# Kernel optimization log

Measured on AMD Instinct MI355X. Metric: run time of the kernel, lower is better.

The kernel has to match this reference:

```python
import jax, jax.numpy as jnp
import numpy as np

EPS = 1e-5


def gather_nodes(nodes, idx):
    # nodes: [B,N,C], idx: [B,N,K] -> [B,N,K,C]
    return jax.vmap(lambda n, e: n[e])(nodes, idx)


def layer_norm(x, g, b):
    m = jnp.mean(x, axis=-1, keepdims=True)
    v = jnp.mean((x - m) ** 2, axis=-1, keepdims=True)
    return (x - m) * jax.lax.rsqrt(v + EPS) * g + b


def linear(x, W, b):
    return x @ W + b


def setup_inputs() -> dict:
    key = jax.random.key(0)
    B, N, K, H = 2, 2048, 48, 128
    ks = jax.random.split(key, 32)
    it = iter(range(32))
    def nrm(shape, scale=0.05):
        return jax.random.normal(ks[next(it)], shape, dtype=jnp.float32) * scale
    inp = {
        "h_V": nrm((B, N, H), 1.0),
        "h_V_atom": nrm((B, N, H), 1.0),
        "h_E": nrm((B, N, K, H), 1.0),
        # message MLP 1: in = H + 2*(H+H) = 5H = 640
        "W1": nrm((5 * H, H)), "b1": jnp.zeros((H,), jnp.float32),
        "W2": nrm((H, H)), "b2": jnp.zeros((H,), jnp.float32),
        "W3": nrm((H, H)), "b3": jnp.zeros((H,), jnp.float32),
        # message MLP 2: in = H + (H+H) = 3H = 384
        "W11": nrm((3 * H, H)), "b11": jnp.zeros((H,), jnp.float32),
        "W12": nrm((H, H)), "b12": jnp.zeros((H,), jnp.float32),
        "W13": nrm((H, H)), "b13": jnp.zeros((H,), jnp.float32),
        # FFN
        "W_in": nrm((H, 4 * H)), "b_in": jnp.zeros((4 * H,), jnp.float32),
        "W_out": nrm((4 * H, H)), "b_out": jnp.zeros((H,), jnp.float32),
        # LayerNorms
        "g1": jnp.ones((H,), jnp.float32), "be1": jnp.zeros((H,), jnp.float32),
        "g2": jnp.ones((H,), jnp.float32), "be2": jnp.zeros((H,), jnp.float32),
        "g3": jnp.ones((H,), jnp.float32), "be3": jnp.zeros((H,), jnp.float32),
        "mask_V": jnp.ones((B, N), jnp.float32),
        "mask_attend": jnp.ones((B, N, K), jnp.float32),
        "E_idx": jax.random.randint(ks[next(it)], (B, N, K), 0, N),
    }
    return inp


def reference(h_V, h_V_atom, h_E, W1, b1, W2, b2, W3, b3, W11, b11, W12, b12,
              W13, b13, W_in, b_in, W_out, b_out, g1, be1, g2, be2, g3, be3,
              mask_V, mask_attend, E_idx):
    gelu = lambda x: jax.nn.gelu(x, approximate=False)
    SCALE = 30.0
    K = h_E.shape[-2]

    # --- node message ---
    h_EV = jnp.concatenate([
        jnp.broadcast_to(h_V[:, :, None, :], h_E.shape[:3] + (h_V.shape[-1],)),
        h_E, gather_nodes(h_V, E_idx),
        h_E, gather_nodes(h_V_atom, E_idx),
    ], axis=-1)  # [B,N,K,5H]
    h_message = linear(gelu(linear(gelu(linear(h_EV, W1, b1)), W2, b2)), W3, b3)
    h_message = mask_attend[..., None] * h_message
    dh = jnp.sum(h_message, axis=-2) / SCALE
    h_V = layer_norm(h_V + dh, g1, be1)

    # --- FFN ---
    dh = linear(gelu(linear(h_V, W_in, b_in)), W_out, b_out)
    h_V = layer_norm(h_V + dh, g2, be2)
    h_V = mask_V[..., None] * h_V

    # --- edge update ---
    h_EV2 = jnp.concatenate([
        jnp.broadcast_to(h_V[:, :, None, :], h_E.shape[:3] + (h_V.shape[-1],)),
        h_E, gather_nodes(h_V, E_idx),
    ], axis=-1)  # [B,N,K,3H]
    h_message = linear(gelu(linear(gelu(linear(h_EV2, W11, b11)), W12, b12)), W13, b13)
    h_E = layer_norm(h_E + h_message, g3, be3)
    return (h_V, h_E)
```

## Files before the change

### kernel.cpp

```cpp
#include <hip/hip_runtime.h>
#include <hip/hip_bf16.h>

#define H 128
#define NN 2048
#define BB 2
#define EPSF 1e-5f

typedef __bf16 bf16;
typedef bf16 bf16x8 __attribute__((ext_vector_type(8)));
typedef bf16 bf16x4 __attribute__((ext_vector_type(4)));
typedef float f32x4 __attribute__((ext_vector_type(4)));
typedef float f32x2 __attribute__((ext_vector_type(2)));

#define U1_F     155648
#define U2_F     679936
#define HVMID_F  1204224
#define V2_F     1990656
#define V1_F     2252800
#define HVMID_B  3457024

__device__ __forceinline__ float gelu_f(float x) {
    float u = x * x;
    float p = __builtin_fmaf(u, 0.044715f, 1.0f);
    float w = x * p;
    float e = __builtin_amdgcn_exp2f(w * -2.3022083f);
    return x * __builtin_amdgcn_rcpf(1.0f + e);
}

#define MFMA16(a, b, c) __builtin_amdgcn_mfma_f32_16x16x32_bf16((a), (b), (c), 0, 0, 0)

#define GEMM_PIPE(U, A_EXPR, B0p, B1p, ACC)                                       \
    {                                                                             \
        bf16x8 bq0[3], bq1[3];                                                    \
        _Pragma("unroll")                                                         \
        for (int j = 0; j < 3 && j < (U); ++j) {                                  \
            bq0[j] = *(const bf16x8*)((B0p) + j * 32);                            \
            bq1[j] = *(const bf16x8*)((B1p) + j * 32);                            \
        }                                                                         \
        bf16x8 afc[3], afn[3];                                                    \
        _Pragma("unroll")                                                         \
        for (int rt = 0; rt < 3; ++rt) { const int u = 0; afc[rt] = (A_EXPR); }   \
        _Pragma("unroll")                                                         \
        for (int uu = 0; uu < (U); ++uu) {                                        \
            if (uu + 1 < (U)) {                                                   \
                _Pragma("unroll")                                                 \
                for (int rt = 0; rt < 3; ++rt) { const int u = uu + 1; afn[rt] = (A_EXPR); } \
            }                                                                     \
            __builtin_amdgcn_s_setprio(1);                                        \
            _Pragma("unroll")                                                     \
            for (int rt = 0; rt < 3; ++rt) {                                      \
                ACC[rt][0] = MFMA16(afc[rt], bq0[uu % 3], ACC[rt][0]);            \
                ACC[rt][1] = MFMA16(afc[rt], bq1[uu % 3], ACC[rt][1]);            \
            }                                                                     \
            __builtin_amdgcn_s_setprio(0);                                        \
            if (uu + 3 < (U)) {                                                   \
                bq0[uu % 3] = *(const bf16x8*)((B0p) + (uu + 3) * 32);            \
                bq1[uu % 3] = *(const bf16x8*)((B1p) + (uu + 3) * 32);            \
            }                                                                     \
            _Pragma("unroll")                                                     \
            for (int rt = 0; rt < 3; ++rt) afc[rt] = afn[rt];                     \
        }                                                                         \
    }

#define PACK_STORE(DST, ROW, PCOL, V0, V1)                                        \
    {                                                                             \
        union { bf16 h[2]; unsigned u; } pk_;                                     \
        pk_.h[0] = (V0); pk_.h[1] = (V1);                                         \
        *(unsigned*)&DST[ROW][PCOL] = pk_.u;                                      \
    }

__global__ void prep_weights(const float* __restrict__ W1, const float* __restrict__ W2,
                             const float* __restrict__ W3, const float* __restrict__ W11,
                             const float* __restrict__ W12, const float* __restrict__ W13,
                             const float* __restrict__ Win, const float* __restrict__ Wout,
                             bf16* __restrict__ ws)
{
    int i = blockIdx.x * 256 + threadIdx.x;
    float v;
    if (i < 65536) {
        int c = i >> 9, k = i & 511, s = k >> 7, k0 = k & 127;
        if (s == 0)      v = W1[k0 * H + c];
        else if (s == 1) {
            int klog = (k0 & ~31) + ((k0 & 1) << 4) + ((k0 & 31) >> 1);
            v = W1[(128 + klog) * H + c] + W1[(384 + klog) * H + c];
        }
        else if (s == 2) v = W1[(256 + k0) * H + c];
        else             v = W1[(512 + k0) * H + c];
    } else if (i < 81920)  { int j = i - 65536;  int c = j >> 7, p = j & 127;
                             int k = (p & ~31) + ((p & 1) << 4) + ((p & 31) >> 1);
                             v = W2[k * H + c]; }
    else if (i < 98304)    { int j = i - 81920;  int c = j >> 7, p = j & 127;
                             int k = (p & ~31) + ((p & 1) << 4) + ((p & 31) >> 1);
                             v = W3[k * H + c]; }
    else if (i < 147456)   { int j = i - 98304;  int c = j / 384, k = j - c * 384;
                             if (k >= 128 && k < 256) {
                                 int p = k - 128;
                                 int klog = (p & ~31) + ((p & 1) << 4) + ((p & 31) >> 1);
                                 v = W11[(128 + klog) * H + c];
                             } else {
                                 v = W11[k * H + c];
                             } }
    else if (i < 163840)   { int j = i - 147456; int c = j >> 7, p = j & 127;
                             int k = (p & ~31) + ((p & 1) << 4) + ((p & 31) >> 1);
                             v = W12[k * H + c]; }
    else if (i < 180224)   { int j = i - 163840; int c = j >> 7, p = j & 127;
                             int k = (p & ~31) + ((p & 1) << 4) + ((p & 31) >> 1);
                             v = W13[k * H + c]; }
    else if (i < 245760)   { int j = i - 180224; int jj = j >> 7, k = j & 127; v = Win[k * 512 + jj]; }
    else                   { int j = i - 245760; int c = j >> 9, k = j & 511; v = Wout[k * H + c]; }
    ws[i] = (bf16)v;
}

__global__ __launch_bounds__(512) void u1_kernel(
    const float* __restrict__ hV, const float* __restrict__ hVa,
    const float* __restrict__ b1, const bf16* __restrict__ ws, float* __restrict__ wsf)
{
    int n0 = blockIdx.x * 128;
    int t = threadIdx.x, w = t >> 6, l = t & 63, l16 = l & 15, lg = l >> 4;
    int wm = w >> 2, wn = w & 3;
    __shared__ __align__(16) bf16 sA[128][136];
    __shared__ __align__(16) bf16 sB[128][136];

    #pragma unroll
    for (int i = 0; i < 8; ++i) {
        int idx = t + i * 512;
        int row = idx >> 5, c4 = (idx & 31) << 2;
        f32x4 v = *(const f32x4*)(hV + (size_t)(n0 + row) * H + c4);
        bf16x4 o; o[0] = (bf16)v[0]; o[1] = (bf16)v[1]; o[2] = (bf16)v[2]; o[3] = (bf16)v[3];
        *(bf16x4*)(&sA[row][c4]) = o;
        f32x4 va = *(const f32x4*)(hVa + (size_t)(n0 + row) * H + c4);
        bf16x4 oa; oa[0] = (bf16)va[0]; oa[1] = (bf16)va[1]; oa[2] = (bf16)va[2]; oa[3] = (bf16)va[3];
        *(bf16x4*)(&sB[row][c4]) = oa;
    }
    __syncthreads();

    f32x4 accU[4][2], accV[4][2];
    #pragma unroll
    for (int rt = 0; rt < 4; ++rt)
        #pragma unroll
        for (int c2 = 0; c2 < 2; ++c2) {
            accU[rt][c2] = (f32x4){0.f, 0.f, 0.f, 0.f};
            accV[rt][c2] = (f32x4){0.f, 0.f, 0.f, 0.f};
        }
    #pragma unroll
    for (int kk = 0; kk < 4; ++kk) {
        bf16x8 af[4];
        #pragma unroll
        for (int rt = 0; rt < 4; ++rt)
            af[rt] = *(const bf16x8*)(&sA[wm * 64 + rt * 16 + l16][kk * 32 + lg * 8]);
        #pragma unroll
        for (int c2 = 0; c2 < 2; ++c2) {
            int c = wn * 32 + c2 * 16 + l16;
            bf16x8 bU = *(const bf16x8*)(&ws[(size_t)c * 512 + kk * 32 + lg * 8]);
            bf16x8 bV = *(const bf16x8*)(&ws[(size_t)c * 512 + 256 + kk * 32 + lg * 8]);
            #pragma unroll
            for (int rt = 0; rt < 4; ++rt) {
                accU[rt][c2] = MFMA16(af[rt], bU, accU[rt][c2]);
                accV[rt][c2] = MFMA16(af[rt], bV, accV[rt][c2]);
            }
        }
    }
    #pragma unroll
    for (int kk = 0; kk < 4; ++kk) {
        bf16x8 af[4];
        #pragma unroll
        for (int rt = 0; rt < 4; ++rt)
            af[rt] = *(const bf16x8*)(&sB[wm * 64 + rt * 16 + l16][kk * 32 + lg * 8]);
        #pragma unroll
        for (int c2 = 0; c2 < 2; ++c2) {
            int c = wn * 32 + c2 * 16 + l16;
            bf16x8 bV = *(const bf16x8*)(&ws[(size_t)c * 512 + 384 + kk * 32 + lg * 8]);
            #pragma unroll
            for (int rt = 0; rt < 4; ++rt)
                accV[rt][c2] = MFMA16(af[rt], bV, accV[rt][c2]);
        }
    }
    {
        int col0 = wn * 32 + l16, col1 = col0 + 16;
        int pcol = wn * 32 + l16 * 2;
        float bb0 = b1[col0], bb1 = b1[col1];
        #pragma unroll
        for (int rt = 0; rt < 4; ++rt)
            #pragma unroll
            for (int i = 0; i < 4; ++i) {
                int row = wm * 64 + rt * 16 + lg * 4 + i;
                f32x2 su; su[0] = accU[rt][0][i] + bb0; su[1] = accU[rt][1][i] + bb1;
                *(f32x2*)(wsf + U1_F + (size_t)(n0 + row) * H + pcol) = su;
                f32x2 sv; sv[0] = accV[rt][0][i]; sv[1] = accV[rt][1][i];
                *(f32x2*)(wsf + V1_F + (size_t)(n0 + row) * H + pcol) = sv;
            }
    }
}

__global__ __launch_bounds__(256, 4) void node_msg_kernel(
    const float* __restrict__ hV, const float* __restrict__ hE,
    const float* __restrict__ b2, const float* __restrict__ b3,
    const float* __restrict__ g1, const float* __restrict__ be1,
    const float* __restrict__ maskA, const int* __restrict__ Eidx,
    bf16* __restrict__ ws, float* __restrict__ wsf)
{
    __shared__ __align__(16) char smem[27136];
    bf16 (*sA)[136]  = (bf16(*)[136])smem;
    bf16 (*sH1)[136] = (bf16(*)[136])smem;
    bf16 (*sH2)[136] = (bf16(*)[136])(smem + 13056);
    float* sDH = (float*)(smem + 26112);

    int n = blockIdx.x, b = n >> 11;
    int t = threadIdx.x, w = t >> 6, l = t & 63, l16 = l & 15, lg = l >> 4;

    int col0 = w * 32 + l16, col1 = col0 + 16;
    int pcol = w * 32 + l16 * 2;
    f32x2 u1p = *(const f32x2*)(wsf + U1_F + (size_t)n * H + pcol);
    float b2v0 = b2[col0], b2v1 = b2[col1];
    float b3v0 = b3[col0], b3v1 = b3[col1];

    float v1v0[3][4], v1v1[3][4];
    #pragma unroll
    for (int rt = 0; rt < 3; ++rt)
        #pragma unroll
        for (int i = 0; i < 4; ++i) {
            int row = rt * 16 + lg * 4 + i;
            int nbr = Eidx[n * 48 + row];
            f32x2 vv = *(const f32x2*)(wsf + V1_F + ((size_t)b * NN + nbr) * H + pcol);
            v1v0[rt][i] = vv[0];
            v1v1[rt][i] = vv[1];
        }

    #pragma unroll
    for (int i = 0; i < 6; ++i) {
        int idx = t + i * 256;
        int row = idx >> 5, q = idx & 31;
        int c0 = (q >> 3) * 32 + (q & 7) * 2;
        const float* hp = hE + ((size_t)n * 48 + row) * H + c0;
        f32x2 a = *(const f32x2*)(hp);
        f32x2 c = *(const f32x2*)(hp + 16);
        bf16x4 o; o[0] = (bf16)a[0]; o[1] = (bf16)c[0]; o[2] = (bf16)a[1]; o[3] = (bf16)c[1];
        *(bf16x4*)(&sA[row][q * 4]) = o;
    }
    __syncthreads();

    f32x4 acc[3][2];
    #pragma unroll
    for (int rt = 0; rt < 3; ++rt)
        #pragma unroll
        for (int c2 = 0; c2 < 2; ++c2) acc[rt][c2] = (f32x4){0.f, 0.f, 0.f, 0.f};
    {
        const bf16* B0 = ws + (size_t)col0 * 512 + 128 + lg * 8;
        const bf16* B1 = ws + (size_t)col1 * 512 + 128 + lg * 8;
        GEMM_PIPE(4, (*(const bf16x8*)(&sA[rt * 16 + l16][u * 32 + lg * 8])), B0, B1, acc)
    }
    __syncthreads();

    #pragma unroll
    for (int rt = 0; rt < 3; ++rt)
        #pragma unroll
        for (int i = 0; i < 4; ++i) {
            int row = rt * 16 + lg * 4 + i;
            bf16 v0 = (bf16)gelu_f(acc[rt][0][i] + u1p[0] + v1v0[rt][i]);
            bf16 v1 = (bf16)gelu_f(acc[rt][1][i] + u1p[1] + v1v1[rt][i]);
            PACK_STORE(sH1, row, pcol, v0, v1)
        }
    __syncthreads();

    f32x4 a2[3][2];
    #pragma unroll
    for (int rt = 0; rt < 3; ++rt)
        #pragma unroll
        for (int c2 = 0; c2 < 2; ++c2) a2[rt][c2] = (f32x4){0.f, 0.f, 0.f, 0.f};
    {
        const bf16* B0 = ws + 65536 + (size_t)col0 * 128 + lg * 8;
        const bf16* B1 = ws + 65536 + (size_t)col1 * 128 + lg * 8;
        GEMM_PIPE(4, (*(const bf16x8*)(&sH1[rt * 16 + l16][u * 32 + lg * 8])), B0, B1, a2)
    }
    #pragma unroll
    for (int rt = 0; rt < 3; ++rt)
        #pragma unroll
        for (int i = 0; i < 4; ++i) {
            int row = rt * 16 + lg * 4 + i;
            bf16 v0 = (bf16)gelu_f(a2[rt][0][i] + b2v0);
            bf16 v1 = (bf16)gelu_f(a2[rt][1][i] + b2v1);
            PACK_STORE(sH2, row, pcol, v0, v1)
        }
    __syncthreads();

    float mk[3][4];
    #pragma unroll
    for (int rt = 0; rt < 3; ++rt)
        #pragma unroll
        for (int i = 0; i < 4; ++i)
            mk[rt][i] = maskA[n * 48 + rt * 16 + lg * 4 + i];

    f32x4 a3[3][2];
    #pragma unroll
    for (int rt = 0; rt < 3; ++rt)
        #pragma unroll
        for (int c2 = 0; c2 < 2; ++c2) a3[rt][c2] = (f32x4){0.f, 0.f, 0.f, 0.f};
    {
        const bf16* B0 = ws + 81920 + (size_t)col0 * 128 + lg * 8;
        const bf16* B1 = ws + 81920 + (size_t)col1 * 128 + lg * 8;
        GEMM_PIPE(4, (*(const bf16x8*)(&sH2[rt * 16 + l16][u * 32 + lg * 8])), B0, B1, a3)
    }
    float r0s = 0.f, r1s = 0.f;
    #pragma unroll
    for (int rt = 0; rt < 3; ++rt)
        #pragma unroll
        for (int i = 0; i < 4; ++i) {
            r0s += (a3[rt][0][i] + b3v0) * mk[rt][i];
            r1s += (a3[rt][1][i] + b3v1) * mk[rt][i];
        }
    r0s += __shfl_xor(r0s, 16); r0s += __shfl_xor(r0s, 32);
    r1s += __shfl_xor(r1s, 16); r1s += __shfl_xor(r1s, 32);
    if (l < 16) { sDH[w * 32 + l] = r0s; sDH[w * 32 + 16 + l] = r1s; }
    __syncthreads();

    if (w == 0) {
        float x0 = hV[(size_t)n * H + l] + sDH[l] * (1.0f / 30.0f);
        float x1 = hV[(size_t)n * H + l + 64] + sDH[l + 64] * (1.0f / 30.0f);
        float s1 = x0 + x1, s2 = x0 * x0 + x1 * x1;
        #pragma unroll
        for (int off = 32; off; off >>= 1) { s1 += __shfl_xor(s1, off); s2 += __shfl_xor(s2, off); }
        float m = s1 * (1.f / 128.f);
        float rs = rsqrtf(s2 * (1.f / 128.f) - m * m + EPSF);
        float y0 = (x0 - m) * rs * g1[l] + be1[l];
        float y1 = (x1 - m) * rs * g1[l + 64] + be1[l + 64];
        wsf[HVMID_F + (size_t)n * H + l] = y0;
        wsf[HVMID_F + (size_t)n * H + l + 64] = y1;
        ws[HVMID_B + (size_t)n * H + l] = (bf16)y0;
        ws[HVMID_B + (size_t)n * H + l + 64] = (bf16)y1;
    }
}

__global__ __launch_bounds__(512) void ffn_kernel(
    const float* __restrict__ b_in, const float* __restrict__ b_out,
    const float* __restrict__ b11, const float* __restrict__ g2,
    const float* __restrict__ be2, const float* __restrict__ maskV,
    bf16* __restrict__ ws, float* __restrict__ wsf, float* __restrict__ outV)
{
    int n0 = blockIdx.x * 32;
    int t = threadIdx.x, w = t >> 6, l = t & 63, l16 = l & 15, lg = l >> 4;

    __shared__ __align__(16) char smem[8704 + 33280];
    bf16 (*sA)[136]  = (bf16(*)[136])(smem);
    bf16 (*sFF)[520] = (bf16(*)[520])(smem + 8704);
    float (*sX)[132] = (float(*)[132])(smem + 8704);

    {
        int row = t >> 4, c8 = (t & 15) << 3;
        *(bf16x8*)(&sA[row][c8]) = *(const bf16x8*)(ws + HVMID_B + (size_t)(n0 + row) * H + c8);
    }
    __syncthreads();

    f32x4 a1[2][4];
    #pragma unroll
    for (int rt = 0; rt < 2; ++rt)
        #pragma unroll
        for (int ct = 0; ct < 4; ++ct) a1[rt][ct] = (f32x4){0.f, 0.f, 0.f, 0.f};
    #pragma unroll
    for (int kk = 0; kk < 4; ++kk) {
        bf16x8 af[2];
        #pragma unroll
        for (int rt = 0; rt < 2; ++rt)
            af[rt] = *(const bf16x8*)(&sA[rt * 16 + l16][kk * 32 + lg * 8]);
        #pragma unroll
        for (int ct = 0; ct < 4; ++ct) {
            int c = w * 64 + ct * 16 + l16;
            bf16x8 bfr = *(const bf16x8*)(&ws[180224 + (size_t)c * 128 + kk * 32 + lg * 8]);
            #pragma unroll
            for (int rt = 0; rt < 2; ++rt)
                a1[rt][ct] = MFMA16(af[rt], bfr, a1[rt][ct]);
        }
    }
    #pragma unroll
    for (int ct = 0; ct < 4; ++ct) {
        int c = w * 64 + ct * 16 + l16;
        float bb = b_in[c];
        #pragma unroll
        for (int rt = 0; rt < 2; ++rt)
            #pragma unroll
            for (int i = 0; i < 4; ++i) {
                int row = rt * 16 + lg * 4 + i;
                sFF[row][c] = (bf16)gelu_f(a1[rt][ct][i] + bb);
            }
    }
    __syncthreads();

    f32x4 a2[2];
    a2[0] = (f32x4){0.f, 0.f, 0.f, 0.f}; a2[1] = (f32x4){0.f, 0.f, 0.f, 0.f};
    int cc = w * 16 + l16;
    #pragma unroll
    for (int kk = 0; kk < 16; ++kk) {
        bf16x8 af[2];
        #pragma unroll
        for (int rt = 0; rt < 2; ++rt)
            af[rt] = *(const bf16x8*)(&sFF[rt * 16 + l16][kk * 32 + lg * 8]);
        bf16x8 bfr = *(const bf16x8*)(&ws[245760 + (size_t)cc * 512 + kk * 32 + lg * 8]);
        #pragma unroll
        for (int rt = 0; rt < 2; ++rt)
            a2[rt] = MFMA16(af[rt], bfr, a2[rt]);
    }
    __syncthreads();
    {
        float bb = b_out[cc];
        #pragma unroll
        for (int rt = 0; rt < 2; ++rt)
            #pragma unroll
            for (int i = 0; i < 4; ++i) {
                int row = rt * 16 + lg * 4 + i;
                sX[row][cc] = a2[rt][i] + bb + wsf[HVMID_F + (size_t)(n0 + row) * H + cc];
            }
    }
    __syncthreads();

    if (t < 128) {
        int row = t >> 2, q = t & 3;
        float xr[32], s1 = 0.f, s2 = 0.f;
        #pragma unroll
        for (int j = 0; j < 32; ++j) {
            float x = sX[row][q * 32 + j];
            xr[j] = x; s1 += x; s2 += x * x;
        }
        s1 += __shfl_xor(s1, 1); s1 += __shfl_xor(s1, 2);
        s2 += __shfl_xor(s2, 1); s2 += __shfl_xor(s2, 2);
        float m = s1 * (1.f / 128.f);
        float vv = s2 * (1.f / 128.f) - m * m;
        float rs = rsqrtf(vv + EPSF);
        float mv = maskV[n0 + row];
        #pragma unroll
        for (int j = 0; j < 32; ++j) {
            int c = q * 32 + j;
            float y = ((xr[j] - m) * rs * g2[c] + be2[c]) * mv;
            outV[(size_t)(n0 + row) * H + c] = y;
            sA[row][c] = (bf16)y;
        }
    }
    __syncthreads();

    f32x4 a3[2], a4[2];
    a3[0] = (f32x4){0.f, 0.f, 0.f, 0.f}; a3[1] = (f32x4){0.f, 0.f, 0.f, 0.f};
    a4[0] = (f32x4){0.f, 0.f, 0.f, 0.f}; a4[1] = (f32x4){0.f, 0.f, 0.f, 0.f};
    #pragma unroll
    for (int kk = 0; kk < 4; ++kk) {
        bf16x8 af[2];
        #pragma unroll
        for (int rt = 0; rt < 2; ++rt)
            af[rt] = *(const bf16x8*)(&sA[rt * 16 + l16][kk * 32 + lg * 8]);
        bf16x8 bU = *(const bf16x8*)(&ws[98304 + (size_t)cc * 384 + kk * 32 + lg * 8]);
        bf16x8 bV = *(const bf16x8*)(&ws[98304 + (size_t)cc * 384 + 256 + kk * 32 + lg * 8]);
        #pragma unroll
        for (int rt = 0; rt < 2; ++rt) {
            a3[rt] = MFMA16(af[rt], bU, a3[rt]);
            a4[rt] = MFMA16(af[rt], bV, a4[rt]);
        }
    }
    {
        float bb = b11[cc];
        int pc = (cc & ~31) + l16 * 2 + ((cc >> 4) & 1);
        #pragma unroll
        for (int rt = 0; rt < 2; ++rt)
            #pragma unroll
            for (int i = 0; i < 4; ++i) {
                int row = rt * 16 + lg * 4 + i;
                wsf[U2_F + (size_t)(n0 + row) * H + pc] = a3[rt][i] + bb;
                wsf[V2_F + (size_t)(n0 + row) * H + pc] = a4[rt][i];
            }
    }
}

__global__ __launch_bounds__(256, 4) void edge_kernel(
    const float* __restrict__ hE, const float* __restrict__ b12,
    const float* __restrict__ b13, const float* __restrict__ g3,
    const float* __restrict__ be3, const int* __restrict__ Eidx,
    const bf16* __restrict__ ws, const float* __restrict__ wsf,
    float* __restrict__ outE)
{
    __shared__ __align__(16) char smem[26112];
    bf16 (*sA)[136]  = (bf16(*)[136])smem;
    bf16 (*sH1)[136] = (bf16(*)[136])smem;
    bf16 (*sH2)[136] = (bf16(*)[136])(smem + 13056);
    float (*sP1)[4]  = (float(*)[4])smem;
    float (*sP2)[4]  = (float(*)[4])(smem + 1024);

    int n = blockIdx.x, b = n >> 11;
    int t = threadIdx.x, w = t >> 6, l = t & 63, l16 = l & 15, lg = l >> 4;

    int col0 = w * 32 + l16, col1 = col0 + 16;
    int pcol = w * 32 + l16 * 2;
    f32x2 u2p = *(const f32x2*)(wsf + U2_F + (size_t)n * H + pcol);
    float b12v0 = b12[col0], b12v1 = b12[col1];
    float b13v0 = b13[col0], b13v1 = b13[col1];
    float g3v0 = g3[col0], g3v1 = g3[col1];
    float be3v0 = be3[col0], be3v1 = be3[col1];

    float v2v0[3][4], v2v1[3][4];
    #pragma unroll
    for (int rt = 0; rt < 3; ++rt)
        #pragma unroll
        for (int i = 0; i < 4; ++i) {
            int row = rt * 16 + lg * 4 + i;
            int nbr = Eidx[n * 48 + row];
            f32x2 vv = *(const f32x2*)(wsf + V2_F + ((size_t)b * NN + nbr) * H + pcol);
            v2v0[rt][i] = vv[0];
            v2v1[rt][i] = vv[1];
        }

    #pragma unroll
    for (int i = 0; i < 6; ++i) {
        int idx = t + i * 256;
        int row = idx >> 5, q = idx & 31;
        int c0 = (q >> 3) * 32 + (q & 7) * 2;
        const float* hp = hE + ((size_t)n * 48 + row) * H + c0;
        f32x2 a = *(const f32x2*)(hp);
        f32x2 c = *(const f32x2*)(hp + 16);
        bf16x4 o; o[0] = (bf16)a[0]; o[1] = (bf16)c[0]; o[2] = (bf16)a[1]; o[3] = (bf16)c[1];
        *(bf16x4*)(&sA[row][q * 4]) = o;
    }
    __syncthreads();

    f32x4 acc[3][2];
    #pragma unroll
    for (int rt = 0; rt < 3; ++rt)
        #pragma unroll
        for (int c2 = 0; c2 < 2; ++c2) acc[rt][c2] = (f32x4){0.f, 0.f, 0.f, 0.f};
    {
        const bf16* B0 = ws + 98304 + (size_t)col0 * 384 + 128 + lg * 8;
        const bf16* B1 = ws + 98304 + (size_t)col1 * 384 + 128 + lg * 8;
        GEMM_PIPE(4, (*(const bf16x8*)(&sA[rt * 16 + l16][u * 32 + lg * 8])), B0, B1, acc)
    }

    float rv0[3][4], rv1[3][4];
    #pragma unroll
    for (int rt = 0; rt < 3; ++rt)
        #pragma unroll
        for (int i = 0; i < 4; ++i) {
            union { unsigned u; bf16 h[2]; } rp;
            rp.u = *(const unsigned*)&sA[rt * 16 + lg * 4 + i][pcol];
            rv0[rt][i] = (float)rp.h[0];
            rv1[rt][i] = (float)rp.h[1];
        }
    __syncthreads();

    #pragma unroll
    for (int rt = 0; rt < 3; ++rt)
        #pragma unroll
        for (int i = 0; i < 4; ++i) {
            int row = rt * 16 + lg * 4 + i;
            bf16 v0 = (bf16)gelu_f(acc[rt][0][i] + u2p[0] + v2v0[rt][i]);
            bf16 v1 = (bf16)gelu_f(acc[rt][1][i] + u2p[1] + v2v1[rt][i]);
            PACK_STORE(sH1, row, pcol, v0, v1)
        }
    __syncthreads();

    f32x4 a2[3][2];
    #pragma unroll
    for (int rt = 0; rt < 3; ++rt)
        #pragma unroll
        for (int c2 = 0; c2 < 2; ++c2) a2[rt][c2] = (f32x4){0.f, 0.f, 0.f, 0.f};
    {
        const bf16* B0 = ws + 147456 + (size_t)col0 * 128 + lg * 8;
        const bf16* B1 = ws + 147456 + (size_t)col1 * 128 + lg * 8;
        GEMM_PIPE(4, (*(const bf16x8*)(&sH1[rt * 16 + l16][u * 32 + lg * 8])), B0, B1, a2)
    }
    #pragma unroll
    for (int rt = 0; rt < 3; ++rt)
        #pragma unroll
        for (int i = 0; i < 4; ++i) {
            int row = rt * 16 + lg * 4 + i;
            bf16 v0 = (bf16)gelu_f(a2[rt][0][i] + b12v0);
            bf16 v1 = (bf16)gelu_f(a2[rt][1][i] + b12v1);
            PACK_STORE(sH2, row, pcol, v0, v1)
        }
    __syncthreads();

    f32x4 a3[3][2];
    #pragma unroll
    for (int rt = 0; rt < 3; ++rt)
        #pragma unroll
        for (int c2 = 0; c2 < 2; ++c2) a3[rt][c2] = (f32x4){0.f, 0.f, 0.f, 0.f};
    {
        const bf16* B0 = ws + 163840 + (size_t)col0 * 128 + lg * 8;
        const bf16* B1 = ws + 163840 + (size_t)col1 * 128 + lg * 8;
        GEMM_PIPE(4, (*(const bf16x8*)(&sH2[rt * 16 + l16][u * 32 + lg * 8])), B0, B1, a3)
    }

    float s1r[3][4], s2r[3][4];
    #pragma unroll
    for (int rt = 0; rt < 3; ++rt)
        #pragma unroll
        for (int i = 0; i < 4; ++i) { s1r[rt][i] = 0.f; s2r[rt][i] = 0.f; }
    #pragma unroll
    for (int rt = 0; rt < 3; ++rt)
        #pragma unroll
        for (int i = 0; i < 4; ++i) {
            float v0 = a3[rt][0][i] + b13v0 + rv0[rt][i];
            float v1 = a3[rt][1][i] + b13v1 + rv1[rt][i];
            a3[rt][0][i] = v0; a3[rt][1][i] = v1;
            s1r[rt][i] = v0 + v1; s2r[rt][i] = v0 * v0 + v1 * v1;
        }
    #pragma unroll
    for (int mseg = 1; mseg < 16; mseg <<= 1)
        #pragma unroll
        for (int rt = 0; rt < 3; ++rt)
            #pragma unroll
            for (int i = 0; i < 4; ++i) {
                s1r[rt][i] += __shfl_xor(s1r[rt][i], mseg);
                s2r[rt][i] += __shfl_xor(s2r[rt][i], mseg);
            }
    if (l16 == 0) {
        #pragma unroll
        for (int rt = 0; rt < 3; ++rt)
            #pragma unroll
            for (int i = 0; i < 4; ++i) {
                int row = rt * 16 + lg * 4 + i;
                sP1[row][w] = s1r[rt][i];
                sP2[row][w] = s2r[rt][i];
            }
    }
    __syncthreads();

    #pragma unroll
    for (int rt = 0; rt < 3; ++rt)
        #pragma unroll
        for (int i = 0; i < 4; ++i) {
            int row = rt * 16 + lg * 4 + i;
            f32x4 p1 = *(const f32x4*)sP1[row];
            f32x4 p2 = *(const f32x4*)sP2[row];
            float s1 = p1[0] + p1[1] + p1[2] + p1[3];
            float s2 = p2[0] + p2[1] + p2[2] + p2[3];
            float mn = s1 * (1.f / 128.f);
            float rs = rsqrtf(s2 * (1.f / 128.f) - mn * mn + EPSF);
            size_t rb = ((size_t)n * 48 + row) * H;
            outE[rb + col0] = (a3[rt][0][i] - mn) * rs * g3v0 + be3v0;
            outE[rb + col1] = (a3[rt][1][i] - mn) * rs * g3v1 + be3v1;
        }
}

extern "C" void kernel_launch(void* const* d_in, const int* in_sizes, int n_in,
                              void* d_out, int out_size, void* d_ws, size_t ws_size,
                              hipStream_t stream)
{
    const float* hV    = (const float*)d_in[0];
    const float* hVa   = (const float*)d_in[1];
    const float* hE    = (const float*)d_in[2];
    const float* W1    = (const float*)d_in[3];
    const float* b1    = (const float*)d_in[4];
    const float* W2    = (const float*)d_in[5];
    const float* b2    = (const float*)d_in[6];
    const float* W3    = (const float*)d_in[7];
    const float* b3    = (const float*)d_in[8];
    const float* W11   = (const float*)d_in[9];
    const float* b11   = (const float*)d_in[10];
    const float* W12   = (const float*)d_in[11];
    const float* b12   = (const float*)d_in[12];
    const float* W13   = (const float*)d_in[13];
    const float* b13   = (const float*)d_in[14];
    const float* Win   = (const float*)d_in[15];
    const float* b_in  = (const float*)d_in[16];
    const float* Wout  = (const float*)d_in[17];
    const float* b_out = (const float*)d_in[18];
    const float* g1    = (const float*)d_in[19];
    const float* be1   = (const float*)d_in[20];
    const float* g2    = (const float*)d_in[21];
    const float* be2   = (const float*)d_in[22];
    const float* g3    = (const float*)d_in[23];
    const float* be3   = (const float*)d_in[24];
    const float* maskV = (const float*)d_in[25];
    const float* maskA = (const float*)d_in[26];
    const int*   Eidx  = (const int*)  d_in[27];

    bf16*  ws   = (bf16*)d_ws;
    float* wsf  = (float*)d_ws;
    float* outV = (float*)d_out;
    float* outE = outV + (size_t)BB * NN * H;

    prep_weights<<<1216, 256, 0, stream>>>(W1, W2, W3, W11, W12, W13, Win, Wout, ws);
    u1_kernel<<<32, 512, 0, stream>>>(hV, hVa, b1, ws, wsf);
    node_msg_kernel<<<BB * NN, 256, 0, stream>>>(hV, hE, b2, b3, g1, be1, maskA, Eidx, ws, wsf);
    ffn_kernel<<<BB * NN / 32, 512, 0, stream>>>(b_in, b_out, b11, g2, be2, maskV, ws, wsf, outV);
    edge_kernel<<<BB * NN, 256, 0, stream>>>(hE, b12, b13, g3, be3, Eidx, ws, wsf, outE);
}
```

Baseline: 176.5 us.

## Process four nodes per block with double-buffered prefetch of next node's edges

Node-message and edge kernels now handle four nodes per block in a loop, double-buffering the bf16 edge tile in shared memory and prefetching the next node's h_E, U/V gathers, and neighbor indices into registers while the current node's GEMMs run. This amortizes per-block setup (bias/gamma loads) and hides global load latency behind MFMA work. In exchange, shared memory and register use grow (launch bounds drop to 3 blocks/SM) and the grid shrinks to 1024 blocks, reducing parallelism.

```diff
diff --git a/kernel.cpp b/kernel.cpp
--- a/kernel.cpp
+++ b/kernel.cpp
@@ -5,6 +5,7 @@
 #define NN 2048
 #define BB 2
 #define EPSF 1e-5f
+#define NPER 4
 
 typedef __bf16 bf16;
 typedef bf16 bf16x8 __attribute__((ext_vector_type(8)));
@@ -192,141 +193,190 @@
     }
 }
 
-__global__ __launch_bounds__(256, 4) void node_msg_kernel(
+__global__ __launch_bounds__(256, 3) void node_msg_kernel(
     const float* __restrict__ hV, const float* __restrict__ hE,
     const float* __restrict__ b2, const float* __restrict__ b3,
     const float* __restrict__ g1, const float* __restrict__ be1,
     const float* __restrict__ maskA, const int* __restrict__ Eidx,
     bf16* __restrict__ ws, float* __restrict__ wsf)
 {
-    __shared__ __align__(16) char smem[27136];
-    bf16 (*sA)[136]  = (bf16(*)[136])smem;
-    bf16 (*sH1)[136] = (bf16(*)[136])smem;
-    bf16 (*sH2)[136] = (bf16(*)[136])(smem + 13056);
-    float* sDH = (float*)(smem + 26112);
-
-    int n = blockIdx.x, b = n >> 11;
+    __shared__ __align__(16) char smem[40192];
+    bf16 (*sH2)[136] = (bf16(*)[136])(smem + 26112);
+    float* sDH = (float*)(smem + 39168);
+
     int t = threadIdx.x, w = t >> 6, l = t & 63, l16 = l & 15, lg = l >> 4;
-
     int col0 = w * 32 + l16, col1 = col0 + 16;
     int pcol = w * 32 + l16 * 2;
-    f32x2 u1p = *(const f32x2*)(wsf + U1_F + (size_t)n * H + pcol);
     float b2v0 = b2[col0], b2v1 = b2[col1];
     float b3v0 = b3[col0], b3v1 = b3[col1];
 
-    float v1v0[3][4], v1v1[3][4];
+    int n0b = blockIdx.x * NPER, b = n0b >> 11;
+
+    f32x2 u1p = *(const f32x2*)(wsf + U1_F + (size_t)n0b * H + pcol);
+    float v1a[3][4], v1b[3][4];
     #pragma unroll
     for (int rt = 0; rt < 3; ++rt)
         #pragma unroll
         for (int i = 0; i < 4; ++i) {
             int row = rt * 16 + lg * 4 + i;
-            int nbr = Eidx[n * 48 + row];
+            int nbr = Eidx[n0b * 48 + row];
             f32x2 vv = *(const f32x2*)(wsf + V1_F + ((size_t)b * NN + nbr) * H + pcol);
-            v1v0[rt][i] = vv[0];
-            v1v1[rt][i] = vv[1];
-        }
-
-    #pragma unroll
-    for (int i = 0; i < 6; ++i) {
-        int idx = t + i * 256;
-        int row = idx >> 5, q = idx & 31;
-        int c0 = (q >> 3) * 32 + (q & 7) * 2;
-        const float* hp = hE + ((size_t)n * 48 + row) * H + c0;
-        f32x2 a = *(const f32x2*)(hp);
-        f32x2 c = *(const f32x2*)(hp + 16);
-        bf16x4 o; o[0] = (bf16)a[0]; o[1] = (bf16)c[0]; o[2] = (bf16)a[1]; o[3] = (bf16)c[1];
-        *(bf16x4*)(&sA[row][q * 4]) = o;
+            v1a[rt][i] = vv[0]; v1b[rt][i] = vv[1];
+        }
+    {
+        bf16 (*sA0)[136] = (bf16(*)[136])smem;
+        #pragma unroll
+        for (int i = 0; i < 6; ++i) {
+            int idx = t + i * 256, row = idx >> 5, q = idx & 31;
+            int c0 = (q >> 3) * 32 + (q & 7) * 2;
+            const float* hp = hE + ((size_t)n0b * 48 + row) * H + c0;
+            f32x2 a = *(const f32x2*)hp, c = *(const f32x2*)(hp + 16);
+            bf16x4 o; o[0] = (bf16)a[0]; o[1] = (bf16)c[0]; o[2] = (bf16)a[1]; o[3] = (bf16)c[1];
+            *(bf16x4*)(&sA0[row][q * 4]) = o;
+        }
     }
     __syncthreads();
 
-    f32x4 acc[3][2];
-    #pragma unroll
-    for (int rt = 0; rt < 3; ++rt)
-        #pragma unroll
-        for (int c2 = 0; c2 < 2; ++c2) acc[rt][c2] = (f32x4){0.f, 0.f, 0.f, 0.f};
-    {
-        const bf16* B0 = ws + (size_t)col0 * 512 + 128 + lg * 8;
-        const bf16* B1 = ws + (size_t)col1 * 512 + 128 + lg * 8;
-        GEMM_PIPE(4, (*(const bf16x8*)(&sA[rt * 16 + l16][u * 32 + lg * 8])), B0, B1, acc)
-    }
-    __syncthreads();
-
-    #pragma unroll
-    for (int rt = 0; rt < 3; ++rt)
-        #pragma unroll
-        for (int i = 0; i < 4; ++i) {
-            int row = rt * 16 + lg * 4 + i;
-            bf16 v0 = (bf16)gelu_f(acc[rt][0][i] + u1p[0] + v1v0[rt][i]);
-            bf16 v1 = (bf16)gelu_f(acc[rt][1][i] + u1p[1] + v1v1[rt][i]);
-            PACK_STORE(sH1, row, pcol, v0, v1)
-        }
-    __syncthreads();
-
-    f32x4 a2[3][2];
-    #pragma unroll
-    for (int rt = 0; rt < 3; ++rt)
-        #pragma unroll
-        for (int c2 = 0; c2 < 2; ++c2) a2[rt][c2] = (f32x4){0.f, 0.f, 0.f, 0.f};
-    {
-        const bf16* B0 = ws + 65536 + (size_t)col0 * 128 + lg * 8;
-        const bf16* B1 = ws + 65536 + (size_t)col1 * 128 + lg * 8;
-        GEMM_PIPE(4, (*(const bf16x8*)(&sH1[rt * 16 + l16][u * 32 + lg * 8])), B0, B1, a2)
-    }
-    #pragma unroll
-    for (int rt = 0; rt < 3; ++rt)
-        #pragma unroll
-        for (int i = 0; i < 4; ++i) {
-            int row = rt * 16 + lg * 4 + i;
-            bf16 v0 = (bf16)gelu_f(a2[rt][0][i] + b2v0);
-            bf16 v1 = (bf16)gelu_f(a2[rt][1][i] + b2v1);
-            PACK_STORE(sH2, row, pcol, v0, v1)
-        }
-    __syncthreads();
-
-    float mk[3][4];
-    #pragma unroll
-    for (int rt = 0; rt < 3; ++rt)
-        #pragma unroll
-        for (int i = 0; i < 4; ++i)
-            mk[rt][i] = maskA[n * 48 + rt * 16 + lg * 4 + i];
-
-    f32x4 a3[3][2];
-    #pragma unroll
-    for (int rt = 0; rt < 3; ++rt)
-        #pragma unroll
-        for (int c2 = 0; c2 < 2; ++c2) a3[rt][c2] = (f32x4){0.f, 0.f, 0.f, 0.f};
-    {
-        const bf16* B0 = ws + 81920 + (size_t)col0 * 128 + lg * 8;
-        const bf16* B1 = ws + 81920 + (size_t)col1 * 128 + lg * 8;
-        GEMM_PIPE(4, (*(const bf16x8*)(&sH2[rt * 16 + l16][u * 32 + lg * 8])), B0, B1, a3)
-    }
-    float r0s = 0.f, r1s = 0.f;
-    #pragma unroll
-    for (int rt = 0; rt < 3; ++rt)
-        #pragma unroll
-        for (int i = 0; i < 4; ++i) {
-            r0s += (a3[rt][0][i] + b3v0) * mk[rt][i];
-            r1s += (a3[rt][1][i] + b3v1) * mk[rt][i];
-        }
-    r0s += __shfl_xor(r0s, 16); r0s += __shfl_xor(r0s, 32);
-    r1s += __shfl_xor(r1s, 16); r1s += __shfl_xor(r1s, 32);
-    if (l < 16) { sDH[w * 32 + l] = r0s; sDH[w * 32 + 16 + l] = r1s; }
-    __syncthreads();
-
-    if (w == 0) {
-        float x0 = hV[(size_t)n * H + l] + sDH[l] * (1.0f / 30.0f);
-        float x1 = hV[(size_t)n * H + l + 64] + sDH[l + 64] * (1.0f / 30.0f);
-        float s1 = x0 + x1, s2 = x0 * x0 + x1 * x1;
-        #pragma unroll
-        for (int off = 32; off; off >>= 1) { s1 += __shfl_xor(s1, off); s2 += __shfl_xor(s2, off); }
-        float m = s1 * (1.f / 128.f);
-        float rs = rsqrtf(s2 * (1.f / 128.f) - m * m + EPSF);
-        float y0 = (x0 - m) * rs * g1[l] + be1[l];
-        float y1 = (x1 - m) * rs * g1[l + 64] + be1[l + 64];
-        wsf[HVMID_F + (size_t)n * H + l] = y0;
-        wsf[HVMID_F + (size_t)n * H + l + 64] = y1;
-        ws[HVMID_B + (size_t)n * H + l] = (bf16)y0;
-        ws[HVMID_B + (size_t)n * H + l + 64] = (bf16)y1;
+    int cur = 0;
+    #pragma unroll 1
+    for (int it = 0; it < NPER; ++it) {
+        int n = n0b + it;
+        bf16 (*sA)[136]  = (bf16(*)[136])(smem + cur * 13056);
+        bf16 (*sAn)[136] = (bf16(*)[136])(smem + (cur ^ 1) * 13056);
+
+        f32x2 nga[6], ngc[6];
+        if (it + 1 < NPER) {
+            #pragma unroll
+            for (int i = 0; i < 6; ++i) {
+                int idx = t + i * 256, row = idx >> 5, q = idx & 31;
+                int c0 = (q >> 3) * 32 + (q & 7) * 2;
+                const float* hp = hE + ((size_t)(n + 1) * 48 + row) * H + c0;
+                nga[i] = *(const f32x2*)hp; ngc[i] = *(const f32x2*)(hp + 16);
+            }
+        }
+
+        f32x4 acc[3][2];
+        #pragma unroll
+        for (int rt = 0; rt < 3; ++rt)
+            #pragma unroll
+            for (int c2 = 0; c2 < 2; ++c2) acc[rt][c2] = (f32x4){0.f, 0.f, 0.f, 0.f};
+        {
+            const bf16* B0 = ws + (size_t)col0 * 512 + 128 + lg * 8;
+            const bf16* B1 = ws + (size_t)col1 * 512 + 128 + lg * 8;
+            GEMM_PIPE(4, (*(const bf16x8*)(&sA[rt * 16 + l16][u * 32 + lg * 8])), B0, B1, acc)
+        }
+        __syncthreads();
+
+        #pragma unroll
+        for (int rt = 0; rt < 3; ++rt)
+            #pragma unroll
+            for (int i = 0; i < 4; ++i) {
+                int row = rt * 16 + lg * 4 + i;
+                bf16 v0 = (bf16)gelu_f(acc[rt][0][i] + u1p[0] + v1a[rt][i]);
+                bf16 v1 = (bf16)gelu_f(acc[rt][1][i] + u1p[1] + v1b[rt][i]);
+                PACK_STORE(sA, row, pcol, v0, v1)
+            }
+
+        if (it + 1 < NPER) {
+            #pragma unroll
+            for (int i = 0; i < 6; ++i) {
+                int idx = t + i * 256, row = idx >> 5, q = idx & 31;
+                bf16x4 o; o[0] = (bf16)nga[i][0]; o[1] = (bf16)ngc[i][0];
+                o[2] = (bf16)nga[i][1]; o[3] = (bf16)ngc[i][1];
+                *(bf16x4*)(&sAn[row][q * 4]) = o;
+            }
+        }
+
+        float mk[3][4];
+        #pragma unroll
+        for (int rt = 0; rt < 3; ++rt)
+            #pragma unroll
+            for (int i = 0; i < 4; ++i)
+                mk[rt][i] = maskA[n * 48 + rt * 16 + lg * 4 + i];
+        f32x2 u1pn; float v1an[3][4], v1bn[3][4];
+        if (it + 1 < NPER) {
+            u1pn = *(const f32x2*)(wsf + U1_F + (size_t)(n + 1) * H + pcol);
+            #pragma unroll
+            for (int rt = 0; rt < 3; ++rt)
+                #pragma unroll
+                for (int i = 0; i < 4; ++i) {
+                    int row = rt * 16 + lg * 4 + i;
+                    int nbr = Eidx[(n + 1) * 48 + row];
+                    f32x2 vv = *(const f32x2*)(wsf + V1_F + ((size_t)b * NN + nbr) * H + pcol);
+                    v1an[rt][i] = vv[0]; v1bn[rt][i] = vv[1];
+                }
+        }
+        __syncthreads();
+
+        f32x4 a2[3][2];
+        #pragma unroll
+        for (int rt = 0; rt < 3; ++rt)
+            #pragma unroll
+            for (int c2 = 0; c2 < 2; ++c2) a2[rt][c2] = (f32x4){0.f, 0.f, 0.f, 0.f};
+        {
+            const bf16* B0 = ws + 65536 + (size_t)col0 * 128 + lg * 8;
+            const bf16* B1 = ws + 65536 + (size_t)col1 * 128 + lg * 8;
+            GEMM_PIPE(4, (*(const bf16x8*)(&sA[rt * 16 + l16][u * 32 + lg * 8])), B0, B1, a2)
+        }
+        #pragma unroll
+        for (int rt = 0; rt < 3; ++rt)
+            #pragma unroll
+            for (int i = 0; i < 4; ++i) {
+                int row = rt * 16 + lg * 4 + i;
+                bf16 v0 = (bf16)gelu_f(a2[rt][0][i] + b2v0);
+                bf16 v1 = (bf16)gelu_f(a2[rt][1][i] + b2v1);
+                PACK_STORE(sH2, row, pcol, v0, v1)
+            }
+        __syncthreads();
+
+        f32x4 a3[3][2];
+        #pragma unroll
+        for (int rt = 0; rt < 3; ++rt)
+            #pragma unroll
+            for (int c2 = 0; c2 < 2; ++c2) a3[rt][c2] = (f32x4){0.f, 0.f, 0.f, 0.f};
+        {
+            const bf16* B0 = ws + 81920 + (size_t)col0 * 128 + lg * 8;
+            const bf16* B1 = ws + 81920 + (size_t)col1 * 128 + lg * 8;
+            GEMM_PIPE(4, (*(const bf16x8*)(&sH2[rt * 16 + l16][u * 32 + lg * 8])), B0, B1, a3)
+        }
+        float r0s = 0.f, r1s = 0.f;
+        #pragma unroll
+        for (int rt = 0; rt < 3; ++rt)
+            #pragma unroll
+            for (int i = 0; i < 4; ++i) {
+                r0s += (a3[rt][0][i] + b3v0) * mk[rt][i];
+                r1s += (a3[rt][1][i] + b3v1) * mk[rt][i];
+            }
+        r0s += __shfl_xor(r0s, 16); r0s += __shfl_xor(r0s, 32);
+        r1s += __shfl_xor(r1s, 16); r1s += __shfl_xor(r1s, 32);
+        if (l < 16) { sDH[w * 32 + l] = r0s; sDH[w * 32 + 16 + l] = r1s; }
+        __syncthreads();
+
+        if (w == 0) {
+            float x0 = hV[(size_t)n * H + l] + sDH[l] * (1.0f / 30.0f);
+            float x1 = hV[(size_t)n * H + l + 64] + sDH[l + 64] * (1.0f / 30.0f);
+            float s1 = x0 + x1, s2 = x0 * x0 + x1 * x1;
+            #pragma unroll
+            for (int off = 32; off; off >>= 1) { s1 += __shfl_xor(s1, off); s2 += __shfl_xor(s2, off); }
+            float m = s1 * (1.f / 128.f);
+            float rs = rsqrtf(s2 * (1.f / 128.f) - m * m + EPSF);
+            float y0 = (x0 - m) * rs * g1[l] + be1[l];
+            float y1 = (x1 - m) * rs * g1[l + 64] + be1[l + 64];
+            wsf[HVMID_F + (size_t)n * H + l] = y0;
+            wsf[HVMID_F + (size_t)n * H + l + 64] = y1;
+            ws[HVMID_B + (size_t)n * H + l] = (bf16)y0;
+            ws[HVMID_B + (size_t)n * H + l + 64] = (bf16)y1;
+        }
+
+        if (it + 1 < NPER) {
+            u1p = u1pn;
+            #pragma unroll
+            for (int rt = 0; rt < 3; ++rt)
+                #pragma unroll
+                for (int i = 0; i < 4; ++i) { v1a[rt][i] = v1an[rt][i]; v1b[rt][i] = v1bn[rt][i]; }
+        }
+        cur ^= 1;
+        __syncthreads();
     }
 }
 
@@ -466,172 +516,214 @@
     }
 }
 
-__global__ __launch_bounds__(256, 4) void edge_kernel(
+__global__ __launch_bounds__(256, 3) void edge_kernel(
     const float* __restrict__ hE, const float* __restrict__ b12,
     const float* __restrict__ b13, const float* __restrict__ g3,
     const float* __restrict__ be3, const int* __restrict__ Eidx,
     const bf16* __restrict__ ws, const float* __restrict__ wsf,
     float* __restrict__ outE)
 {
-    __shared__ __align__(16) char smem[26112];
-    bf16 (*sA)[136]  = (bf16(*)[136])smem;
-    bf16 (*sH1)[136] = (bf16(*)[136])smem;
-    bf16 (*sH2)[136] = (bf16(*)[136])(smem + 13056);
-    float (*sP1)[4]  = (float(*)[4])smem;
-    float (*sP2)[4]  = (float(*)[4])(smem + 1024);
-
-    int n = blockIdx.x, b = n >> 11;
+    __shared__ __align__(16) char smem[40704];
+    bf16 (*sH2)[136] = (bf16(*)[136])(smem + 26112);
+    float (*sP1)[4]  = (float(*)[4])(smem + 39168);
+    float (*sP2)[4]  = (float(*)[4])(smem + 39936);
+
     int t = threadIdx.x, w = t >> 6, l = t & 63, l16 = l & 15, lg = l >> 4;
-
     int col0 = w * 32 + l16, col1 = col0 + 16;
     int pcol = w * 32 + l16 * 2;
-    f32x2 u2p = *(const f32x2*)(wsf + U2_F + (size_t)n * H + pcol);
     float b12v0 = b12[col0], b12v1 = b12[col1];
     float b13v0 = b13[col0], b13v1 = b13[col1];
     float g3v0 = g3[col0], g3v1 = g3[col1];
     float be3v0 = be3[col0], be3v1 = be3[col1];
 
-    float v2v0[3][4], v2v1[3][4];
+    int n0b = blockIdx.x * NPER, b = n0b >> 11;
+
+    f32x2 u2p = *(const f32x2*)(wsf + U2_F + (size_t)n0b * H + pcol);
+    float v2a[3][4], v2b[3][4];
     #pragma unroll
     for (int rt = 0; rt < 3; ++rt)
         #pragma unroll
         for (int i = 0; i < 4; ++i) {
             int row = rt * 16 + lg * 4 + i;
-            int nbr = Eidx[n * 48 + row];
+            int nbr = Eidx[n0b * 48 + row];
             f32x2 vv = *(const f32x2*)(wsf + V2_F + ((size_t)b * NN + nbr) * H + pcol);
-            v2v0[rt][i] = vv[0];
-            v2v1[rt][i] = vv[1];
-        }
-
-    #pragma unroll
-    for (int i = 0; i < 6; ++i) {
-        int idx = t + i * 256;
-        int row = idx >> 5, q = idx & 31;
-        int c0 = (q >> 3) * 32 + (q & 7) * 2;
-        const float* hp = hE + ((size_t)n * 48 + row) * H + c0;
-        f32x2 a = *(const f32x2*)(hp);
-        f32x2 c = *(const f32x2*)(hp + 16);
-        bf16x4 o; o[0] = (bf16)a[0]; o[1] = (bf16)c[0]; o[2] = (bf16)a[1]; o[3] = (bf16)c[1];
-        *(bf16x4*)(&sA[row][q * 4]) = o;
+            v2a[rt][i] = vv[0]; v2b[rt][i] = vv[1];
+        }
+    {
+        bf16 (*sA0)[136] = (bf16(*)[136])smem;
+        #pragma unroll
+        for (int i = 0; i < 6; ++i) {
+            int idx = t + i * 256, row = idx >> 5, q = idx & 31;
+            int c0 = (q >> 3) * 32 + (q & 7) * 2;
+            const float* hp = hE + ((size_t)n0b * 48 + row) * H + c0;
+            f32x2 a = *(const f32x2*)hp, c = *(const f32x2*)(hp + 16);
+            bf16x4 o; o[0] = (bf16)a[0]; o[1] = (bf16)c[0]; o[2] = (bf16)a[1]; o[3] = (bf16)c[1];
+            *(bf16x4*)(&sA0[row][q * 4]) = o;
+        }
     }
     __syncthreads();
 
-    f32x4 acc[3][2];
-    #pragma unroll
-    for (int rt = 0; rt < 3; ++rt)
-        #pragma unroll
-        for (int c2 = 0; c2 < 2; ++c2) acc[rt][c2] = (f32x4){0.f, 0.f, 0.f, 0.f};
-    {
-        const bf16* B0 = ws + 98304 + (size_t)col0 * 384 + 128 + lg * 8;
-        const bf16* B1 = ws + 98304 + (size_t)col1 * 384 + 128 + lg * 8;
-        GEMM_PIPE(4, (*(const bf16x8*)(&sA[rt * 16 + l16][u * 32 + lg * 8])), B0, B1, acc)
-    }
-
-    float rv0[3][4], rv1[3][4];
-    #pragma unroll
-    for (int rt = 0; rt < 3; ++rt)
-        #pragma unroll
-        for (int i = 0; i < 4; ++i) {
-            union { unsigned u; bf16 h[2]; } rp;
-            rp.u = *(const unsigned*)&sA[rt * 16 + lg * 4 + i][pcol];
-            rv0[rt][i] = (float)rp.h[0];
-            rv1[rt][i] = (float)rp.h[1];
-        }
-    __syncthreads();
-
-    #pragma unroll
-    for (int rt = 0; rt < 3; ++rt)
-        #pragma unroll
-        for (int i = 0; i < 4; ++i) {
-            int row = rt * 16 + lg * 4 + i;
-            bf16 v0 = (bf16)gelu_f(acc[rt][0][i] + u2p[0] + v2v0[rt][i]);
-            bf16 v1 = (bf16)gelu_f(acc[rt][1][i] + u2p[1] + v2v1[rt][i]);
-            PACK_STORE(sH1, row, pcol, v0, v1)
-        }
-    __syncthreads();
-
-    f32x4 a2[3][2];
-    #pragma unroll
-    for (int rt = 0; rt < 3; ++rt)
-        #pragma unroll
-        for (int c2 = 0; c2 < 2; ++c2) a2[rt][c2] = (f32x4){0.f, 0.f, 0.f, 0.f};
-    {
-        const bf16* B0 = ws + 147456 + (size_t)col0 * 128 + lg * 8;
-        const bf16* B1 = ws + 147456 + (size_t)col1 * 128 + lg * 8;
-        GEMM_PIPE(4, (*(const bf16x8*)(&sH1[rt * 16 + l16][u * 32 + lg * 8])), B0, B1, a2)
-    }
-    #pragma unroll
-    for (int rt = 0; rt < 3; ++rt)
-        #pragma unroll
-        for (int i = 0; i < 4; ++i) {
-            int row = rt * 16 + lg * 4 + i;
-            bf16 v0 = (bf16)gelu_f(a2[rt][0][i] + b12v0);
-            bf16 v1 = (bf16)gelu_f(a2[rt][1][i] + b12v1);
-            PACK_STORE(sH2, row, pcol, v0, v1)
-        }
-    __syncthreads();
-
-    f32x4 a3[3][2];
-    #pragma unroll
-    for (int rt = 0; rt < 3; ++rt)
-        #pragma unroll
-        for (int c2 = 0; c2 < 2; ++c2) a3[rt][c2] = (f32x4){0.f, 0.f, 0.f, 0.f};
-    {
-        const bf16* B0 = ws + 163840 + (size_t)col0 * 128 + lg * 8;
-        const bf16* B1 = ws + 163840 + (size_t)col1 * 128 + lg * 8;
-        GEMM_PIPE(4, (*(const bf16x8*)(&sH2[rt * 16 + l16][u * 32 + lg * 8])), B0, B1, a3)
-    }
-
-    float s1r[3][4], s2r[3][4];
-    #pragma unroll
-    for (int rt = 0; rt < 3; ++rt)
-        #pragma unroll
-        for (int i = 0; i < 4; ++i) { s1r[rt][i] = 0.f; s2r[rt][i] = 0.f; }
-    #pragma unroll
-    for (int rt = 0; rt < 3; ++rt)
-        #pragma unroll
-        for (int i = 0; i < 4; ++i) {
-            float v0 = a3[rt][0][i] + b13v0 + rv0[rt][i];
-            float v1 = a3[rt][1][i] + b13v1 + rv1[rt][i];
-            a3[rt][0][i] = v0; a3[rt][1][i] = v1;
-            s1r[rt][i] = v0 + v1; s2r[rt][i] = v0 * v0 + v1 * v1;
-        }
-    #pragma unroll
-    for (int mseg = 1; mseg < 16; mseg <<= 1)
-        #pragma unroll
-        for (int rt = 0; rt < 3; ++rt)
-            #pragma unroll
-            for (int i = 0; i < 4; ++i) {
-                s1r[rt][i] += __shfl_xor(s1r[rt][i], mseg);
-                s2r[rt][i] += __shfl_xor(s2r[rt][i], mseg);
-            }
-    if (l16 == 0) {
+    int cur = 0;
+    #pragma unroll 1
+    for (int it = 0; it < NPER; ++it) {
+        int n = n0b + it;
+        bf16 (*sA)[136]  = (bf16(*)[136])(smem + cur * 13056);
+        bf16 (*sAn)[136] = (bf16(*)[136])(smem + (cur ^ 1) * 13056);
+
+        f32x2 nga[6], ngc[6];
+        if (it + 1 < NPER) {
+            #pragma unroll
+            for (int i = 0; i < 6; ++i) {
+                int idx = t + i * 256, row = idx >> 5, q = idx & 31;
+                int c0 = (q >> 3) * 32 + (q & 7) * 2;
+                const float* hp = hE + ((size_t)(n + 1) * 48 + row) * H + c0;
+                nga[i] = *(const f32x2*)hp; ngc[i] = *(const f32x2*)(hp + 16);
+            }
+        }
+
+        f32x4 acc[3][2];
+        #pragma unroll
+        for (int rt = 0; rt < 3; ++rt)
+            #pragma unroll
+            for (int c2 = 0; c2 < 2; ++c2) acc[rt][c2] = (f32x4){0.f, 0.f, 0.f, 0.f};
+        {
+            const bf16* B0 = ws + 98304 + (size_t)col0 * 384 + 128 + lg * 8;
+            const bf16* B1 = ws + 98304 + (size_t)col1 * 384 + 128 + lg * 8;
+            GEMM_PIPE(4, (*(const bf16x8*)(&sA[rt * 16 + l16][u * 32 + lg * 8])), B0, B1, acc)
+        }
+        unsigned rvp[3][4];
+        #pragma unroll
+        for (int rt = 0; rt < 3; ++rt)
+            #pragma unroll
+            for (int i = 0; i < 4; ++i)
+                rvp[rt][i] = *(const unsigned*)&sA[rt * 16 + lg * 4 + i][pcol];
+        __syncthreads();
+
         #pragma unroll
         for (int rt = 0; rt < 3; ++rt)
             #pragma unroll
             for (int i = 0; i < 4; ++i) {
                 int row = rt * 16 + lg * 4 + i;
-                sP1[row][w] = s1r[rt][i];
-                sP2[row][w] = s2r[rt][i];
-            }
-    }
-    __syncthreads();
-
-    #pragma unroll
-    for (int rt = 0; rt < 3; ++rt)
-        #pragma unroll
-        for (int i = 0; i < 4; ++i) {
-            int row = rt * 16 + lg * 4 + i;
-            f32x4 p1 = *(const f32x4*)sP1[row];
-            f32x4 p2 = *(const f32x4*)sP2[row];
-            float s1 = p1[0] + p1[1] + p1[2] + p1[3];
-            float s2 = p2[0] + p2[1] + p2[2] + p2[3];
-            float mn = s1 * (1.f / 128.f);
-            float rs = rsqrtf(s2 * (1.f / 128.f) - mn * mn + EPSF);
-            size_t rb = ((size_t)n * 48 + row) * H;
-            outE[rb + col0] = (a3[rt][0][i] - mn) * rs * g3v0 + be3v0;
-            outE[rb + col1] = (a3[rt][1][i] - mn) * rs * g3v1 + be3v1;
-        }
+                bf16 v0 = (bf16)gelu_f(acc[rt][0][i] + u2p[0] + v2a[rt][i]);
+                bf16 v1 = (bf16)gelu_f(acc[rt][1][i] + u2p[1] + v2b[rt][i]);
+                PACK_STORE(sA, row, pcol, v0, v1)
+            }
+
+        if (it + 1 < NPER) {
+            #pragma unroll
+            for (int i = 0; i < 6; ++i) {
+                int idx = t + i * 256, row = idx >> 5, q = idx & 31;
+                bf16x4 o; o[0] = (bf16)nga[i][0]; o[1] = (bf16)ngc[i][0];
+                o[2] = (bf16)nga[i][1]; o[3] = (bf16)ngc[i][1];
+                *(bf16x4*)(&sAn[row][q * 4]) = o;
+            }
+        }
+
+        f32x2 u2pn; float v2an[3][4], v2bn[3][4];
+        if (it + 1 < NPER) {
+            u2pn = *(const f32x2*)(wsf + U2_F + (size_t)(n + 1) * H + pcol);
+            #pragma unroll
+            for (int rt = 0; rt < 3; ++rt)
+                #pragma unroll
+                for (int i = 0; i < 4; ++i) {
+                    int row = rt * 16 + lg * 4 + i;
+                    int nbr = Eidx[(n + 1) * 48 + row];
+                    f32x2 vv = *(const f32x2*)(wsf + V2_F + ((size_t)b * NN + nbr) * H + pcol);
+                    v2an[rt][i] = vv[0]; v2bn[rt][i] = vv[1];
+                }
+        }
+        __syncthreads();
+
+        f32x4 a2[3][2];
+        #pragma unroll
+        for (int rt = 0; rt < 3; ++rt)
+            #pragma unroll
+            for (int c2 = 0; c2 < 2; ++c2) a2[rt][c2] = (f32x4){0.f, 0.f, 0.f, 0.f};
+        {
+            const bf16* B0 = ws + 147456 + (size_t)col0 * 128 + lg * 8;
+            const bf16* B1 = ws + 147456 + (size_t)col1 * 128 + lg * 8;
+            GEMM_PIPE(4, (*(const bf16x8*)(&sA[rt * 16 + l16][u * 32 + lg * 8])), B0, B1, a2)
+        }
+        #pragma unroll
+        for (int rt = 0; rt < 3; ++rt)
+            #pragma unroll
+            for (int i = 0; i < 4; ++i) {
+                int row = rt * 16 + lg * 4 + i;
+                bf16 v0 = (bf16)gelu_f(a2[rt][0][i] + b12v0);
+                bf16 v1 = (bf16)gelu_f(a2[rt][1][i] + b12v1);
+                PACK_STORE(sH2, row, pcol, v0, v1)
+            }
+        __syncthreads();
+
+        f32x4 a3[3][2];
+        #pragma unroll
+        for (int rt = 0; rt < 3; ++rt)
+            #pragma unroll
+            for (int c2 = 0; c2 < 2; ++c2) a3[rt][c2] = (f32x4){0.f, 0.f, 0.f, 0.f};
+        {
+            const bf16* B0 = ws + 163840 + (size_t)col0 * 128 + lg * 8;
+            const bf16* B1 = ws + 163840 + (size_t)col1 * 128 + lg * 8;
+            GEMM_PIPE(4, (*(const bf16x8*)(&sH2[rt * 16 + l16][u * 32 + lg * 8])), B0, B1, a3)
+        }
+
+        float s1r[3][4], s2r[3][4];
+        #pragma unroll
+        for (int rt = 0; rt < 3; ++rt)
+            #pragma unroll
+            for (int i = 0; i < 4; ++i) {
+                union { unsigned u; bf16 h[2]; } rp; rp.u = rvp[rt][i];
+                float v0 = a3[rt][0][i] + b13v0 + (float)rp.h[0];
+                float v1 = a3[rt][1][i] + b13v1 + (float)rp.h[1];
+                a3[rt][0][i] = v0; a3[rt][1][i] = v1;
+                s1r[rt][i] = v0 + v1; s2r[rt][i] = v0 * v0 + v1 * v1;
+            }
+        #pragma unroll
+        for (int mseg = 1; mseg < 16; mseg <<= 1)
+            #pragma unroll
+            for (int rt = 0; rt < 3; ++rt)
+                #pragma unroll
+                for (int i = 0; i < 4; ++i) {
+                    s1r[rt][i] += __shfl_xor(s1r[rt][i], mseg);
+                    s2r[rt][i] += __shfl_xor(s2r[rt][i], mseg);
+                }
+        if (l16 == 0) {
+            #pragma unroll
+            for (int rt = 0; rt < 3; ++rt)
+                #pragma unroll
+                for (int i = 0; i < 4; ++i) {
+                    int row = rt * 16 + lg * 4 + i;
+                    sP1[row][w] = s1r[rt][i];
+                    sP2[row][w] = s2r[rt][i];
+                }
+        }
+        __syncthreads();
+
+        #pragma unroll
+        for (int rt = 0; rt < 3; ++rt)
+            #pragma unroll
+            for (int i = 0; i < 4; ++i) {
+                int row = rt * 16 + lg * 4 + i;
+                f32x4 p1 = *(const f32x4*)sP1[row];
+                f32x4 p2 = *(const f32x4*)sP2[row];
+                float s1 = p1[0] + p1[1] + p1[2] + p1[3];
+                float s2 = p2[0] + p2[1] + p2[2] + p2[3];
+                float mn = s1 * (1.f / 128.f);
+                float rs = rsqrtf(s2 * (1.f / 128.f) - mn * mn + EPSF);
+                size_t rb = ((size_t)n * 48 + row) * H;
+                outE[rb + col0] = (a3[rt][0][i] - mn) * rs * g3v0 + be3v0;
+                outE[rb + col1] = (a3[rt][1][i] - mn) * rs * g3v1 + be3v1;
+            }
+
+        if (it + 1 < NPER) {
+            u2p = u2pn;
+            #pragma unroll
+            for (int rt = 0; rt < 3; ++rt)
+                #pragma unroll
+                for (int i = 0; i < 4; ++i) { v2a[rt][i] = v2an[rt][i]; v2b[rt][i] = v2bn[rt][i]; }
+        }
+        cur ^= 1;
+        __syncthreads();
+    }
 }
 
 extern "C" void kernel_launch(void* const* d_in, const int* in_sizes, int n_in,
@@ -674,7 +766,7 @@
 
     prep_weights<<<1216, 256, 0, stream>>>(W1, W2, W3, W11, W12, W13, Win, Wout, ws);
     u1_kernel<<<32, 512, 0, stream>>>(hV, hVa, b1, ws, wsf);
-    node_msg_kernel<<<BB * NN, 256, 0, stream>>>(hV, hE, b2, b3, g1, be1, maskA, Eidx, ws, wsf);
+    node_msg_kernel<<<BB * NN / NPER, 256, 0, stream>>>(hV, hE, b2, b3, g1, be1, maskA, Eidx, ws, wsf);
     ffn_kernel<<<BB * NN / 32, 512, 0, stream>>>(b_in, b_out, b11, g2, be2, maskV, ws, wsf, outV);
-    edge_kernel<<<BB * NN, 256, 0, stream>>>(hE, b12, b13, g3, be3, Eidx, ws, wsf, outE);
+    edge_kernel<<<BB * NN / NPER, 256, 0, stream>>>(hE, b12, b13, g3, be3, Eidx, ws, wsf, outE);
 }
```

Result: slower. 461.6 us (+161.5%).
